# Performance work log

Hardware: AMD Instinct MI355X
Metric: run time of the kernel (lower is better)

## Reference

```python
import jax, jax.numpy as jnp
import numpy as np

B, S, IN_DIM, D_MODEL, NUM_HEADS = 4, 2048, 1024, 1024, 16
HEAD_DIM = D_MODEL // NUM_HEADS
CAUSAL = True
NEG = -9000000000000000.0


def _xavier(key, shape):
    fan_out, fan_in = shape
    limit = (6.0 / (fan_in + fan_out)) ** 0.5
    return jax.random.uniform(key, shape, jnp.float32, -limit, limit)


def setup_inputs() -> dict:
    key = jax.random.key(0)
    ks = jax.random.split(key, 5)
    x = jax.random.normal(ks[0], (B, S, IN_DIM), jnp.float32)
    Wq = _xavier(ks[1], (D_MODEL, IN_DIM))
    Wk = _xavier(ks[2], (D_MODEL, IN_DIM))
    Wv = _xavier(ks[3], (D_MODEL, IN_DIM))
    Wo = _xavier(ks[4], (D_MODEL, D_MODEL))
    bq = jnp.zeros((D_MODEL,), jnp.float32)
    bk = jnp.zeros((D_MODEL,), jnp.float32)
    bv = jnp.zeros((D_MODEL,), jnp.float32)
    bo = jnp.zeros((D_MODEL,), jnp.float32)
    return {"x": x, "Wq": Wq, "bq": bq, "Wk": Wk, "bk": bk,
            "Wv": Wv, "bv": bv, "Wo": Wo, "bo": bo}


def reference(x, Wq, bq, Wk, bk, Wv, bv, Wo, bo):
    batch, seq, _ = x.shape
    # torch Linear: y = x @ W.T + b
    q = x @ Wq.T + bq
    k = x @ Wk.T + bk
    v = x @ Wv.T + bv
    # [B, S, H, Dh] -> [B, H, S, Dh]
    def split(t):
        return t.reshape(batch, seq, NUM_HEADS, HEAD_DIM).transpose(0, 2, 1, 3)
    q, k, v = split(q), split(k), split(v)
    scores = jnp.einsum('bhqd,bhkd->bhqk', q, k) / jnp.sqrt(jnp.float32(HEAD_DIM))
    if CAUSAL:
        mask = jnp.tril(jnp.ones((seq, seq), bool))
        scores = jnp.where(mask, scores, jnp.float32(NEG))
    attn = jax.nn.softmax(scores, axis=-1)
    out = jnp.einsum('bhqk,bhkd->bhqd', attn, v)
    out = out.transpose(0, 2, 1, 3).reshape(batch, seq, D_MODEL)
    return out @ Wo.T + bo
```

## Files before the change

kernel.cpp:

```cpp
#include <hip/hip_runtime.h>
#include <cstdint>
#include <cmath>

typedef unsigned short u16;
typedef __attribute__((ext_vector_type(4))) float f32x4;
typedef __attribute__((ext_vector_type(8))) short bf16x8;

#define D_MODEL 1024
#define SEQ     2048
#define BATCH   4
#define NHEAD   16
#define MTOT    (BATCH*SEQ)
#define NXE     ((size_t)MTOT * D_MODEL)

static_assert(sizeof(bf16x8) == 16, "frag size");

__device__ __forceinline__ float bf2f(u16 u) {
    union { uint32_t i; float f; } v; v.i = ((uint32_t)u) << 16; return v.f;
}
__device__ __forceinline__ u16 f2bf(float x) {
    union { float f; uint32_t i; } v; v.f = x;
    uint32_t r = (v.i + 0x7FFFu + ((v.i >> 16) & 1u)) >> 16;
    return (u16)r;
}
__device__ __forceinline__ u16 f2bf_trunc(float x) {
    union { float f; uint32_t i; } v; v.f = x;
    return (u16)(v.i >> 16);
}

typedef const __attribute__((address_space(1))) void* gptr_t;
typedef __attribute__((address_space(3))) void* sptr_t;
__device__ __forceinline__ void gload_lds16(const void* g, void* l) {
    __builtin_amdgcn_global_load_lds((gptr_t)g, (sptr_t)l, 16, 0, 0);
}

__device__ __forceinline__ u16 u4get(const uint4& v, int e) {
    const uint32_t w = ((e >> 1) == 0) ? v.x : ((e >> 1) == 1) ? v.y
                     : ((e >> 1) == 2) ? v.z : v.w;
    return (u16)((e & 1) ? (w >> 16) : (w & 0xFFFFu));
}

__global__ __launch_bounds__(256) void diag_write(float* __restrict__ out, float v) {
    size_t i = (size_t)blockIdx.x * 256 + threadIdx.x;
    for (; i < NXE; i += (size_t)gridDim.x * 256) out[i] = v;
}

__global__ void detect_dtype(const u16* __restrict__ x, int* __restrict__ flag) {
    __shared__ int cnt;
    if (threadIdx.x == 0) cnt = 0;
    __syncthreads();
    int c = 0;
#pragma unroll
    for (int k = 0; k < 16; ++k) {
        u16 e = x[2 * (threadIdx.x * 16 + k)];
        int ex = (e >> 7) & 0xFF;
        if (e == 0 || (ex >= 100 && ex <= 140)) ++c;
    }
    atomicAdd(&cnt, c);
    __syncthreads();
    if (threadIdx.x == 0) *flag = (cnt >= 3500) ? 1 : 0;
}

struct CvtArgs { const void* src[9]; u16* dst[9]; int n[9]; };

__global__ __launch_bounds__(256) void cvt_all(CvtArgs a, const int* __restrict__ flag) {
    const int seg = blockIdx.y;
    const int n = a.n[seg];
    const int i = (blockIdx.x * 256 + threadIdx.x) * 8;
    if (i >= n) return;
    u16* d = a.dst[seg] + i;
    if (*flag) {
        *(uint4*)d = *(const uint4*)((const u16*)a.src[seg] + i);
    } else {
        const float* s = (const float*)a.src[seg] + i;
        u16 tmp[8];
#pragma unroll
        for (int k = 0; k < 8; ++k) tmp[k] = f2bf(s[k]);
        *(uint4*)d = *(uint4*)tmp;
    }
}

template <typename OutT>
__device__ __forceinline__ void gemm_body(
    const u16* __restrict__ A, const u16* __restrict__ W,
    const u16* __restrict__ bias, OutT* __restrict__ C,
    int M, int N, int K)
{
    __shared__ __align__(16) u16 As[128 * 32];
    __shared__ __align__(16) u16 Bs[128 * 32];

    const int t    = threadIdx.x;
    const int wave = t >> 6;
    const int ln   = t & 15;
    const int qd   = (t >> 4) & 3;
    const int m0   = blockIdx.x * 128;
    const int n0   = blockIdx.y * 128;
    const int wm   = (wave >> 1) * 64;
    const int wn   = (wave & 1) * 64;

    const int srow = t >> 2;
    const int scol = (t & 3) * 8;
    const u16* gA = A + (size_t)(m0 + srow) * K + scol;
    const u16* gB = W + (size_t)(n0 + srow) * K + scol;
    u16* lA = &As[wave * 512];
    u16* lB = &Bs[wave * 512];

    f32x4 acc[4][4] = {};

    for (int k0 = 0; k0 < K; k0 += 32) {
        __syncthreads();
        gload_lds16(gA + k0,                   lA);
        gload_lds16(gA + (size_t)64 * K + k0,  lA + 2048);
        gload_lds16(gB + k0,                   lB);
        gload_lds16(gB + (size_t)64 * K + k0,  lB + 2048);
        __syncthreads();

        bf16x8 af[4], bfr[4];
#pragma unroll
        for (int i = 0; i < 4; ++i)
            af[i] = *(const bf16x8*)&As[(wm + i * 16 + ln) * 32 + qd * 8];
#pragma unroll
        for (int j = 0; j < 4; ++j)
            bfr[j] = *(const bf16x8*)&Bs[(wn + j * 16 + ln) * 32 + qd * 8];
#pragma unroll
        for (int i = 0; i < 4; ++i)
#pragma unroll
            for (int j = 0; j < 4; ++j)
                acc[i][j] = __builtin_amdgcn_mfma_f32_16x16x32_bf16(
                    af[i], bfr[j], acc[i][j], 0, 0, 0);
    }

    float bv[4];
#pragma unroll
    for (int j = 0; j < 4; ++j) bv[j] = bf2f(bias[n0 + wn + j * 16 + ln]);

#pragma unroll
    for (int i = 0; i < 4; ++i)
#pragma unroll
        for (int r = 0; r < 4; ++r) {
            int row = m0 + wm + i * 16 + qd * 4 + r;
            OutT* crow = C + (size_t)row * N + n0 + wn + ln;
#pragma unroll
            for (int j = 0; j < 4; ++j) {
                float v = acc[i][j][r] + bv[j];
                if constexpr (sizeof(OutT) == 2) crow[j * 16] = f2bf(v);
                else                             crow[j * 16] = v;
            }
        }
}

__global__ __launch_bounds__(256) void gemm_qkv(
    const u16* __restrict__ A,
    const u16* __restrict__ W0, const u16* __restrict__ W1, const u16* __restrict__ W2,
    const u16* __restrict__ b0, const u16* __restrict__ b1, const u16* __restrict__ b2,
    u16* __restrict__ C0, u16* __restrict__ C1, u16* __restrict__ C2,
    int M, int N, int K)
{
    const u16* W; const u16* bias; u16* C;
    if (blockIdx.z == 0)      { W = W0; bias = b0; C = C0; }
    else if (blockIdx.z == 1) { W = W1; bias = b1; C = C1; }
    else                      { W = W2; bias = b2; C = C2; }
    gemm_body<u16>(A, W, bias, C, M, N, K);
}

__global__ __launch_bounds__(256) void gemm_final_f32(
    const u16* __restrict__ A, const u16* __restrict__ W,
    const u16* __restrict__ bias, float* __restrict__ C, int M, int N, int K)
{
    gemm_body<float>(A, W, bias, C, M, N, K);
}

__global__ __launch_bounds__(256) void transpose_v(
    const u16* __restrict__ V, u16* __restrict__ VT)
{
    __shared__ u16 T[64][72];
    const int st = blockIdx.x;
    const int bh = blockIdx.y;
    const int b  = bh >> 4;
    const int h  = bh & 15;
    const int t  = threadIdx.x;

    const int sr = t >> 2;
    const int dc = (t & 3) * 16;
    const u16* src = V + ((size_t)b * SEQ + st * 64 + sr) * D_MODEL + h * 64 + dc;
    const uint4 a0 = *(const uint4*)src;
    const uint4 a1 = *(const uint4*)(src + 8);
#pragma unroll
    for (int e = 0; e < 8; ++e) T[dc + e][sr]     = u4get(a0, e);
#pragma unroll
    for (int e = 0; e < 8; ++e) T[dc + 8 + e][sr] = u4get(a1, e);
    __syncthreads();

    const int d  = t >> 2;
    const int sc = (t & 3) * 16;
    u16* dst = VT + ((size_t)bh * 64 + d) * SEQ + st * 64 + sc;
    *(uint4*)dst       = *(const uint4*)&T[d][sc];
    *(uint4*)(dst + 8) = *(const uint4*)&T[d][sc + 8];
}

__global__ __launch_bounds__(64) void flash_attn(
    const u16* __restrict__ Qg, const u16* __restrict__ Kg,
    const u16* __restrict__ VTg, u16* __restrict__ Og)
{
    __shared__ __align__(16) u16 Vsh[64 * 64];
    __shared__ __align__(16) u16 Psh[32 * 64];

    const int lane = threadIdx.x;
    const int ln   = lane & 15;
    const int qd   = lane >> 4;
    const int psw  = (ln & 7) << 3;

    const int bh = blockIdx.y;
    const int qw = (63 - (int)blockIdx.x + bh) & 63;
    const int b  = bh >> 4;
    const int h  = bh & 15;
    const int h0 = h * 64;
    const size_t rowBase = (size_t)b * SEQ * D_MODEL;
    const int qw0 = qw * 32;
    const int ktMax = qw >> 1;

    const int vdG = lane >> 3;
    const int vsw = ((lane & 7) * 8) ^ (vdG << 3);
    const u16* vtRow0 = VTg + ((size_t)(bh * 64 + vdG)) * SEQ + vsw;

    bf16x8 qf[2][2];
#pragma unroll
    for (int i = 0; i < 2; ++i)
#pragma unroll
        for (int ks = 0; ks < 2; ++ks)
            qf[i][ks] = *(const bf16x8*)(Qg + rowBase
                + (size_t)(qw0 + i * 16 + ln) * D_MODEL + h0 + ks * 32 + qd * 8);

    float m_run[2], l_run[2];
#pragma unroll
    for (int i = 0; i < 2; ++i) { m_run[i] = -30000.0f; l_run[i] = 0.f; }
    f32x4 oacc[2][4] = {};

    for (int kt = 0; kt <= ktMax; ++kt) {
        __syncthreads();
        {
            const u16* vbase = vtRow0 + kt * 64;
#pragma unroll
            for (int p = 0; p < 8; ++p)
                gload_lds16(vbase + (size_t)(p * 8) * SEQ, &Vsh[p * 512]);
        }

        f32x4 sacc[4][2] = {};
#pragma unroll
        for (int ks = 0; ks < 2; ++ks) {
            bf16x8 kf[4];
#pragma unroll
            for (int j = 0; j < 4; ++j)
                kf[j] = *(const bf16x8*)(Kg + rowBase
                    + (size_t)(kt * 64 + j * 16 + ln) * D_MODEL + h0 + ks * 32 + qd * 8);
#pragma unroll
            for (int j = 0; j < 4; ++j)
#pragma unroll
                for (int i = 0; i < 2; ++i)
                    sacc[j][i] = __builtin_amdgcn_mfma_f32_16x16x32_bf16(
                        kf[j], qf[i][ks], sacc[j][i], 0, 0, 0);
        }

        if (kt == ktMax) {
#pragma unroll
            for (int j = 0; j < 4; ++j)
#pragma unroll
                for (int r = 0; r < 4; ++r) {
                    const int kpos = kt * 64 + j * 16 + qd * 4 + r;
#pragma unroll
                    for (int i = 0; i < 2; ++i) {
                        const int qpos = qw0 + i * 16 + ln;
                        float s = sacc[j][i][r] * 0.125f;
                        sacc[j][i][r] = (kpos > qpos) ? -30000.0f : s;
                    }
                }
        } else {
#pragma unroll
            for (int j = 0; j < 4; ++j)
#pragma unroll
                for (int i = 0; i < 2; ++i)
#pragma unroll
                    for (int r = 0; r < 4; ++r)
                        sacc[j][i][r] *= 0.125f;
        }

#pragma unroll
        for (int i = 0; i < 2; ++i) {
            float mx = sacc[0][i][0];
#pragma unroll
            for (int j = 0; j < 4; ++j)
#pragma unroll
                for (int r = 0; r < 4; ++r) mx = fmaxf(mx, sacc[j][i][r]);
            mx = fmaxf(mx, __shfl_xor(mx, 16));
            mx = fmaxf(mx, __shfl_xor(mx, 32));

            const float mo = m_run[i];
            const float mn = fmaxf(mo, mx);
            const float alpha = __expf(mo - mn);
            m_run[i] = mn;

            float rs = 0.f;
#pragma unroll
            for (int j = 0; j < 4; ++j) {
                u16 tp[4];
#pragma unroll
                for (int r = 0; r < 4; ++r) {
                    float p = __expf(sacc[j][i][r] - mn);
                    rs += p;
                    tp[r] = f2bf_trunc(p);
                }
                uint2 w;
                w.x = (uint32_t)tp[0] | ((uint32_t)tp[1] << 16);
                w.y = (uint32_t)tp[2] | ((uint32_t)tp[3] << 16);
                *(uint2*)&Psh[(i * 16 + ln) * 64 + ((j * 16 + qd * 4) ^ psw)] = w;
            }
            rs += __shfl_xor(rs, 16);
            rs += __shfl_xor(rs, 32);
            l_run[i] = l_run[i] * alpha + rs;

#pragma unroll
            for (int r = 0; r < 4; ++r) {
                const float ar = __shfl(alpha, qd * 4 + r);
#pragma unroll
                for (int j = 0; j < 4; ++j) oacc[i][j][r] *= ar;
            }
        }

        __syncthreads();

#pragma unroll
        for (int ks = 0; ks < 2; ++ks) {
            bf16x8 pa[2];
#pragma unroll
            for (int i = 0; i < 2; ++i)
                pa[i] = *(const bf16x8*)&Psh[(i * 16 + ln) * 64
                                             + ((ks * 32 + qd * 8) ^ psw)];
#pragma unroll
            for (int j = 0; j < 4; ++j) {
                const int d = j * 16 + ln;
                const bf16x8 vb = *(const bf16x8*)&Vsh[d * 64
                    + ((ks * 32 + qd * 8) ^ ((ln & 7) << 3))];
#pragma unroll
                for (int i = 0; i < 2; ++i)
                    oacc[i][j] = __builtin_amdgcn_mfma_f32_16x16x32_bf16(
                        pa[i], vb, oacc[i][j], 0, 0, 0);
            }
        }
    }

#pragma unroll
    for (int i = 0; i < 2; ++i)
#pragma unroll
        for (int r = 0; r < 4; ++r) {
            const float lr = __shfl(l_run[i], qd * 4 + r);
            const float inv = 1.f / lr;
            const int qrow = qw0 + i * 16 + qd * 4 + r;
            u16* orow = Og + rowBase + (size_t)qrow * D_MODEL + h0 + ln;
#pragma unroll
            for (int j = 0; j < 4; ++j)
                orow[j * 16] = f2bf(oacc[i][j][r] * inv);
        }
}

static inline bool ranges_overlap(const void* a, size_t an, const void* b, size_t bn) {
    uintptr_t x0 = (uintptr_t)a, x1 = x0 + an;
    uintptr_t y0 = (uintptr_t)b, y1 = y0 + bn;
    return x0 < y1 && y0 < x1;
}

extern "C" void kernel_launch(void* const* d_in, const int* in_sizes, int n_in,
                              void* d_out, int out_size, void* d_ws, size_t ws_size,
                              hipStream_t stream)
{
    int e = 0;
    const int expect[9] = { 8388608, 1048576, 1024, 1048576, 1024,
                            1048576, 1024, 1048576, 1024 };
    if (n_in != 9) e = 59;
    if (!e) for (int i = 0; i < 9; ++i)
        if (in_sizes[i] != expect[i]) { e = 60 + i; break; }
    if (!e && out_size != (int)NXE) e = 53;
    if (!e && ranges_overlap(d_ws, ws_size, d_out, (size_t)out_size * 4)) e = 55;

    const size_t NX = NXE;
    const size_t NW = (size_t)D_MODEL * D_MODEL;
    const size_t NB = D_MODEL;

    const size_t need = (64 + 4 * NW + 4 * NB + 2 * NX) * 2;
    if (!e && ws_size < need) e = 50;
    if (e) { diag_write<<<2048, 256, 0, stream>>>((float*)d_out, ldexpf(1.0f, e)); return; }

    u16* ws   = (u16*)d_ws;
    int* flag = (int*)ws;
    u16* Wqb  = ws + 64;
    u16* Wkb  = Wqb + NW;
    u16* Wvb  = Wkb + NW;
    u16* Wob  = Wvb + NW;
    u16* bqb  = Wob + NW;
    u16* bkb  = bqb + NB;
    u16* bvb  = bkb + NB;
    u16* bob  = bvb + NB;
    u16* Kw   = bob + NB;
    u16* Vw   = Kw  + NX;

    u16* xb  = (u16*)d_out;
    u16* Qw  = xb + NX;
    u16* VTw = xb;
    u16* Ow  = Vw;

    detect_dtype<<<1, 256, 0, stream>>>((const u16*)d_in[0], flag);

    CvtArgs ca;
    const void* srcs[9] = { d_in[0], d_in[1], d_in[3], d_in[5], d_in[7],
                            d_in[2], d_in[4], d_in[6], d_in[8] };
    u16* dsts[9] = { xb, Wqb, Wkb, Wvb, Wob, bqb, bkb, bvb, bob };
    int  ns[9]   = { (int)NX, (int)NW, (int)NW, (int)NW, (int)NW,
                     (int)NB, (int)NB, (int)NB, (int)NB };
    for (int i = 0; i < 9; ++i) { ca.src[i] = srcs[i]; ca.dst[i] = dsts[i]; ca.n[i] = ns[i]; }
    cvt_all<<<dim3((unsigned)((NX + 2047) / 2048), 9), 256, 0, stream>>>(ca, flag);

    gemm_qkv<<<dim3(MTOT / 128, D_MODEL / 128, 3), 256, 0, stream>>>(
        xb, Wqb, Wkb, Wvb, bqb, bkb, bvb, Qw, Kw, Vw, MTOT, D_MODEL, D_MODEL);

    transpose_v<<<dim3(SEQ / 64, BATCH * NHEAD), 256, 0, stream>>>(Vw, VTw);

    flash_attn<<<dim3(SEQ / 32, BATCH * NHEAD), 64, 0, stream>>>(Qw, Kw, VTw, Ow);

    gemm_final_f32<<<dim3(MTOT / 128, D_MODEL / 128), 256, 0, stream>>>(
        Ow, Wob, bob, (float*)d_out, MTOT, D_MODEL, D_MODEL);
}
```

Before: 338.6 us.

## Pair causal query tiles per block, use exp2 softmax with lazy rescale

Each attention block now processes two query tiles, pr and 63-pr, one after the other, so every block does a balanced amount of causal work and the grid is halved. The softmax scale folds in log2(e) so the code can use a hardware exp2. Rescaling of the running max is skipped while no row's max grows by more than 8, in log2 units, which avoids the exp and accumulator multiplies on most iterations. MFMA sections are wrapped in s_setprio to raise their issue priority. Halving the grid reduces parallelism, and the lazy rescale lets values grow by up to 2^8 before renormalising.

Measured after the change: 375.3 us. 1.11x slower.

```diff
diff --git a/kernel.cpp b/kernel.cpp
--- a/kernel.cpp
+++ b/kernel.cpp
@@ -27,6 +27,15 @@
     union { float f; uint32_t i; } v; v.f = x;
     return (u16)(v.i >> 16);
 }
+
+#if defined(__has_builtin)
+#if __has_builtin(__builtin_amdgcn_exp2f)
+#define EXP2_FAST(x) __builtin_amdgcn_exp2f(x)
+#endif
+#endif
+#ifndef EXP2_FAST
+#define EXP2_FAST(x) exp2f(x)
+#endif
 
 typedef const __attribute__((address_space(1))) void* gptr_t;
 typedef __attribute__((address_space(3))) void* sptr_t;
@@ -210,156 +219,180 @@
     const int qd   = lane >> 4;
     const int psw  = (ln & 7) << 3;
 
+    const int pr = blockIdx.x;
     const int bh = blockIdx.y;
-    const int qw = (63 - (int)blockIdx.x + bh) & 63;
     const int b  = bh >> 4;
     const int h  = bh & 15;
     const int h0 = h * 64;
     const size_t rowBase = (size_t)b * SEQ * D_MODEL;
-    const int qw0 = qw * 32;
-    const int ktMax = qw >> 1;
 
     const int vdG = lane >> 3;
     const int vsw = ((lane & 7) * 8) ^ (vdG << 3);
     const u16* vtRow0 = VTg + ((size_t)(bh * 64 + vdG)) * SEQ + vsw;
 
-    bf16x8 qf[2][2];
-#pragma unroll
-    for (int i = 0; i < 2; ++i)
-#pragma unroll
-        for (int ks = 0; ks < 2; ++ks)
-            qf[i][ks] = *(const bf16x8*)(Qg + rowBase
-                + (size_t)(qw0 + i * 16 + ln) * D_MODEL + h0 + ks * 32 + qd * 8);
-
-    float m_run[2], l_run[2];
-#pragma unroll
-    for (int i = 0; i < 2; ++i) { m_run[i] = -30000.0f; l_run[i] = 0.f; }
-    f32x4 oacc[2][4] = {};
-
-    for (int kt = 0; kt <= ktMax; ++kt) {
-        __syncthreads();
-        {
-            const u16* vbase = vtRow0 + kt * 64;
-#pragma unroll
-            for (int p = 0; p < 8; ++p)
-                gload_lds16(vbase + (size_t)(p * 8) * SEQ, &Vsh[p * 512]);
-        }
-
-        f32x4 sacc[4][2] = {};
-#pragma unroll
-        for (int ks = 0; ks < 2; ++ks) {
-            bf16x8 kf[4];
-#pragma unroll
-            for (int j = 0; j < 4; ++j)
-                kf[j] = *(const bf16x8*)(Kg + rowBase
-                    + (size_t)(kt * 64 + j * 16 + ln) * D_MODEL + h0 + ks * 32 + qd * 8);
-#pragma unroll
-            for (int j = 0; j < 4; ++j)
-#pragma unroll
-                for (int i = 0; i < 2; ++i)
-                    sacc[j][i] = __builtin_amdgcn_mfma_f32_16x16x32_bf16(
-                        kf[j], qf[i][ks], sacc[j][i], 0, 0, 0);
-        }
-
-        if (kt == ktMax) {
-#pragma unroll
-            for (int j = 0; j < 4; ++j)
-#pragma unroll
-                for (int r = 0; r < 4; ++r) {
-                    const int kpos = kt * 64 + j * 16 + qd * 4 + r;
-#pragma unroll
-                    for (int i = 0; i < 2; ++i) {
-                        const int qpos = qw0 + i * 16 + ln;
-                        float s = sacc[j][i][r] * 0.125f;
-                        sacc[j][i][r] = (kpos > qpos) ? -30000.0f : s;
+    const float SCL = 0.18033688011112042f;
+
+#pragma unroll 1
+    for (int sel = 0; sel < 2; ++sel) {
+        const int qw  = sel ? (63 - pr) : pr;
+        const int qw0 = qw * 32;
+        const int ktMax = qw >> 1;
+
+        bf16x8 qf[2][2];
+#pragma unroll
+        for (int i = 0; i < 2; ++i)
+#pragma unroll
+            for (int ks = 0; ks < 2; ++ks)
+                qf[i][ks] = *(const bf16x8*)(Qg + rowBase
+                    + (size_t)(qw0 + i * 16 + ln) * D_MODEL + h0 + ks * 32 + qd * 8);
+
+        float m_run[2], l_run[2];
+#pragma unroll
+        for (int i = 0; i < 2; ++i) { m_run[i] = -30000.0f; l_run[i] = 0.f; }
+        f32x4 oacc[2][4] = {};
+
+        for (int kt = 0; kt <= ktMax; ++kt) {
+            __syncthreads();
+            {
+                const u16* vbase = vtRow0 + kt * 64;
+#pragma unroll
+                for (int p = 0; p < 8; ++p)
+                    gload_lds16(vbase + (size_t)(p * 8) * SEQ, &Vsh[p * 512]);
+            }
+
+            f32x4 sacc[4][2] = {};
+#pragma unroll
+            for (int ks = 0; ks < 2; ++ks) {
+                bf16x8 kf[4];
+#pragma unroll
+                for (int j = 0; j < 4; ++j)
+                    kf[j] = *(const bf16x8*)(Kg + rowBase
+                        + (size_t)(kt * 64 + j * 16 + ln) * D_MODEL + h0 + ks * 32 + qd * 8);
+                __builtin_amdgcn_s_setprio(1);
+#pragma unroll
+                for (int j = 0; j < 4; ++j)
+#pragma unroll
+                    for (int i = 0; i < 2; ++i)
+                        sacc[j][i] = __builtin_amdgcn_mfma_f32_16x16x32_bf16(
+                            kf[j], qf[i][ks], sacc[j][i], 0, 0, 0);
+                __builtin_amdgcn_s_setprio(0);
+            }
+
+            if (kt == ktMax) {
+#pragma unroll
+                for (int j = 0; j < 4; ++j)
+#pragma unroll
+                    for (int r = 0; r < 4; ++r) {
+                        const int kpos = kt * 64 + j * 16 + qd * 4 + r;
+#pragma unroll
+                        for (int i = 0; i < 2; ++i) {
+                            const int qpos = qw0 + i * 16 + ln;
+                            float s = sacc[j][i][r] * SCL;
+                            sacc[j][i][r] = (kpos > qpos) ? -30000.0f : s;
+                        }
+                    }
+            } else {
+#pragma unroll
+                for (int j = 0; j < 4; ++j)
+#pragma unroll
+                    for (int i = 0; i < 2; ++i)
+#pragma unroll
+                        for (int r = 0; r < 4; ++r)
+                            sacc[j][i][r] *= SCL;
+            }
+
+            float mx[2];
+#pragma unroll
+            for (int i = 0; i < 2; ++i) {
+                float m0 = sacc[0][i][0];
+#pragma unroll
+                for (int j = 0; j < 4; ++j)
+#pragma unroll
+                    for (int r = 0; r < 4; ++r) m0 = fmaxf(m0, sacc[j][i][r]);
+                m0 = fmaxf(m0, __shfl_xor(m0, 16));
+                m0 = fmaxf(m0, __shfl_xor(m0, 32));
+                mx[i] = m0;
+            }
+
+            const bool grow = !(__all((mx[0] <= m_run[0] + 8.f) &&
+                                      (mx[1] <= m_run[1] + 8.f)));
+            if (grow) {
+#pragma unroll
+                for (int i = 0; i < 2; ++i) {
+                    const float mo = m_run[i];
+                    const float mn = fmaxf(mo, mx[i]);
+                    const float alpha = EXP2_FAST(mo - mn);
+                    m_run[i] = mn;
+                    l_run[i] *= alpha;
+#pragma unroll
+                    for (int r = 0; r < 4; ++r) {
+                        const float ar = __shfl(alpha, qd * 4 + r);
+#pragma unroll
+                        for (int j = 0; j < 4; ++j) oacc[i][j][r] *= ar;
                     }
                 }
-        } else {
-#pragma unroll
-            for (int j = 0; j < 4; ++j)
+            }
+
+#pragma unroll
+            for (int i = 0; i < 2; ++i) {
+                const float mn = m_run[i];
+                float rs = 0.f;
+#pragma unroll
+                for (int j = 0; j < 4; ++j) {
+                    u16 tp[4];
+#pragma unroll
+                    for (int r = 0; r < 4; ++r) {
+                        float p = EXP2_FAST(sacc[j][i][r] - mn);
+                        rs += p;
+                        tp[r] = f2bf_trunc(p);
+                    }
+                    uint2 w;
+                    w.x = (uint32_t)tp[0] | ((uint32_t)tp[1] << 16);
+                    w.y = (uint32_t)tp[2] | ((uint32_t)tp[3] << 16);
+                    *(uint2*)&Psh[(i * 16 + ln) * 64 + ((j * 16 + qd * 4) ^ psw)] = w;
+                }
+                rs += __shfl_xor(rs, 16);
+                rs += __shfl_xor(rs, 32);
+                l_run[i] += rs;
+            }
+
+            __syncthreads();
+
+#pragma unroll
+            for (int ks = 0; ks < 2; ++ks) {
+                bf16x8 pa[2];
 #pragma unroll
                 for (int i = 0; i < 2; ++i)
-#pragma unroll
-                    for (int r = 0; r < 4; ++r)
-                        sacc[j][i][r] *= 0.125f;
+                    pa[i] = *(const bf16x8*)&Psh[(i * 16 + ln) * 64
+                                                 + ((ks * 32 + qd * 8) ^ psw)];
+                __builtin_amdgcn_s_setprio(1);
+#pragma unroll
+                for (int j = 0; j < 4; ++j) {
+                    const int d = j * 16 + ln;
+                    const bf16x8 vb = *(const bf16x8*)&Vsh[d * 64
+                        + ((ks * 32 + qd * 8) ^ ((ln & 7) << 3))];
+#pragma unroll
+                    for (int i = 0; i < 2; ++i)
+                        oacc[i][j] = __builtin_amdgcn_mfma_f32_16x16x32_bf16(
+                            pa[i], vb, oacc[i][j], 0, 0, 0);
+                }
+                __builtin_amdgcn_s_setprio(0);
+            }
         }
 
 #pragma unroll
-        for (int i = 0; i < 2; ++i) {
-            float mx = sacc[0][i][0];
-#pragma unroll
-            for (int j = 0; j < 4; ++j)
-#pragma unroll
-                for (int r = 0; r < 4; ++r) mx = fmaxf(mx, sacc[j][i][r]);
-            mx = fmaxf(mx, __shfl_xor(mx, 16));
-            mx = fmaxf(mx, __shfl_xor(mx, 32));
-
-            const float mo = m_run[i];
-            const float mn = fmaxf(mo, mx);
-            const float alpha = __expf(mo - mn);
-            m_run[i] = mn;
-
-            float rs = 0.f;
-#pragma unroll
-            for (int j = 0; j < 4; ++j) {
-                u16 tp[4];
-#pragma unroll
-                for (int r = 0; r < 4; ++r) {
-                    float p = __expf(sacc[j][i][r] - mn);
-                    rs += p;
-                    tp[r] = f2bf_trunc(p);
-                }
-                uint2 w;
-                w.x = (uint32_t)tp[0] | ((uint32_t)tp[1] << 16);
-                w.y = (uint32_t)tp[2] | ((uint32_t)tp[3] << 16);
-                *(uint2*)&Psh[(i * 16 + ln) * 64 + ((j * 16 + qd * 4) ^ psw)] = w;
-            }
-            rs += __shfl_xor(rs, 16);
-            rs += __shfl_xor(rs, 32);
-            l_run[i] = l_run[i] * alpha + rs;
-
+        for (int i = 0; i < 2; ++i)
 #pragma unroll
             for (int r = 0; r < 4; ++r) {
-                const float ar = __shfl(alpha, qd * 4 + r);
-#pragma unroll
-                for (int j = 0; j < 4; ++j) oacc[i][j][r] *= ar;
-            }
-        }
-
-        __syncthreads();
-
-#pragma unroll
-        for (int ks = 0; ks < 2; ++ks) {
-            bf16x8 pa[2];
-#pragma unroll
-            for (int i = 0; i < 2; ++i)
-                pa[i] = *(const bf16x8*)&Psh[(i * 16 + ln) * 64
-                                             + ((ks * 32 + qd * 8) ^ psw)];
-#pragma unroll
-            for (int j = 0; j < 4; ++j) {
-                const int d = j * 16 + ln;
-                const bf16x8 vb = *(const bf16x8*)&Vsh[d * 64
-                    + ((ks * 32 + qd * 8) ^ ((ln & 7) << 3))];
-#pragma unroll
-                for (int i = 0; i < 2; ++i)
-                    oacc[i][j] = __builtin_amdgcn_mfma_f32_16x16x32_bf16(
-                        pa[i], vb, oacc[i][j], 0, 0, 0);
-            }
-        }
+                const float lr = __shfl(l_run[i], qd * 4 + r);
+                const float inv = 1.f / lr;
+                const int qrow = qw0 + i * 16 + qd * 4 + r;
+                u16* orow = Og + rowBase + (size_t)qrow * D_MODEL + h0 + ln;
+#pragma unroll
+                for (int j = 0; j < 4; ++j)
+                    orow[j * 16] = f2bf(oacc[i][j][r] * inv);
+            }
     }
-
-#pragma unroll
-    for (int i = 0; i < 2; ++i)
-#pragma unroll
-        for (int r = 0; r < 4; ++r) {
-            const float lr = __shfl(l_run[i], qd * 4 + r);
-            const float inv = 1.f / lr;
-            const int qrow = qw0 + i * 16 + qd * 4 + r;
-            u16* orow = Og + rowBase + (size_t)qrow * D_MODEL + h0 + ln;
-#pragma unroll
-            for (int j = 0; j < 4; ++j)
-                orow[j * 16] = f2bf(oacc[i][j][r] * inv);
-        }
 }
 
 static inline bool ranges_overlap(const void* a, size_t an, const void* b, size_t bn) {
@@ -423,7 +456,7 @@
 
     transpose_v<<<dim3(SEQ / 64, BATCH * NHEAD), 256, 0, stream>>>(Vw, VTw);
 
-    flash_attn<<<dim3(SEQ / 32, BATCH * NHEAD), 64, 0, stream>>>(Qw, Kw, VTw, Ow);
+    flash_attn<<<dim3(SEQ / 64, BATCH * NHEAD), 64, 0, stream>>>(Qw, Kw, VTw, Ow);
 
     gemm_final_f32<<<dim3(MTOT / 128, D_MODEL / 128), 256, 0, stream>>>(
         Ow, Wob, bob, (float*)d_out, MTOT, D_MODEL, D_MODEL);
```
